# Kernel tuning notes

Measured on AMD Instinct MI355X. Metric: run time of the kernel, lower is better.

Reference implementation:

```python
import jax, jax.numpy as jnp
import numpy as np

N, E, F_IN, H, MH, C, G = 100000, 3200000, 128, 32, 64, 10, 64

def _seg_sum(data, ids, num):
    return jax.ops.segment_sum(data, ids, num_segments=num)

def gcn_conv(x, row, col, ew, W, b, n):
    # PyG GCNConv: linear first, then self-loops + symmetric edge-weight norm + scatter-add
    h = x @ W  # [N, H]
    loop = jnp.arange(n)
    r = jnp.concatenate([row, loop])
    c = jnp.concatenate([col, loop])
    w = jnp.concatenate([ew, jnp.ones((n,), dtype=ew.dtype)])
    deg = _seg_sum(w, c, n)
    dinv = jnp.where(deg > 0, jax.lax.rsqrt(deg), 0.0)
    norm = dinv[r] * w * dinv[c]  # [E+N]
    out = _seg_sum(norm[:, None] * h[r], c, n)  # scatter to targets
    return out + b

def setup_inputs():
    key = jax.random.key(0)
    ks = jax.random.split(key, 16)
    inp = {
        "x": jax.random.normal(ks[0], (N, F_IN), dtype=jnp.float32),
        "edge_index": jax.random.randint(ks[1], (2, E), 0, N, dtype=jnp.int64),
        "edge_weight": jax.random.uniform(ks[2], (E,), dtype=jnp.float32),
        "batch": jnp.sort(jax.random.randint(ks[3], (N,), 0, G, dtype=jnp.int64)),
    }
    def lin(k, i, o):
        s = 1.0 / np.sqrt(i)
        k1, k2 = jax.random.split(k)
        return (jax.random.uniform(k1, (i, o), minval=-s, maxval=s, dtype=jnp.float32),
                jax.random.uniform(k2, (o,), minval=-s, maxval=s, dtype=jnp.float32))
    inp["W1"], inp["b1"] = lin(ks[4], F_IN, H)
    inp["W2"], inp["b2"] = lin(ks[5], H, H)
    inp["W3"], inp["b3"] = lin(ks[6], H, H)
    inp["Wm0"], inp["bm0"] = lin(ks[7], H, MH)
    inp["Wm1"], inp["bm1"] = lin(ks[8], MH, MH)
    inp["Wout"], inp["bout"] = lin(ks[9], MH, C)
    return inp

def reference(x, edge_index, edge_weight, batch, W1, b1, W2, b2, W3, b3, Wm0, bm0, Wm1, bm1, Wout, bout):
    row, col = edge_index[0], edge_index[1]
    h = jax.nn.relu(gcn_conv(x, row, col, edge_weight, W1, b1, N))
    h = jax.nn.relu(gcn_conv(h, row, col, edge_weight, W2, b2, N))
    h = gcn_conv(h, row, col, edge_weight, W3, b3, N)
    # global mean pool over graphs
    sums = _seg_sum(h, batch, G)
    counts = _seg_sum(jnp.ones((N,), dtype=h.dtype), batch, G)
    g = sums / jnp.maximum(counts, 1.0)[:, None]
    # dropout p=0.5 is identity at inference (training=False)
    g = jax.nn.relu(g @ Wm0 + bm0)
    g = jax.nn.relu(g @ Wm1 + bm1)
    return g @ Wout + bout
```

## Files before the change

### kernel.cpp

```cpp
#include <hip/hip_runtime.h>

#define NN 100000
#define NE 3200000
#define FIN 128
#define HID 32
#define MH  64
#define NC  10
#define NG  64
#define NBKT 782
#define NBLK 512
#define EPB  (NE / NBLK)
#define SCANL (NBKT * NBLK)
#define SRCMASK 0x1FFFF
#define BCAP 5120

typedef float floatx2 __attribute__((ext_vector_type(2)));

__global__ __launch_bounds__(1024)
void hist_bkt(const int* __restrict__ ei, int* __restrict__ cnt2) {
    __shared__ int h[NBKT];
    int tid = threadIdx.x, blk = blockIdx.x;
    for (int b = tid; b < NBKT; b += 1024) h[b] = 0;
    __syncthreads();
    int base = blk * EPB;
    for (int i = tid; i < EPB; i += 1024)
        atomicAdd(&h[ei[NE + base + i] >> 7], 1);
    __syncthreads();
    for (int b = tid; b < NBKT; b += 1024) cnt2[b * NBLK + blk] = h[b];
}

__global__ void scan_block(const int* __restrict__ in, int* __restrict__ out,
                           int* __restrict__ bsum, int n) {
    __shared__ int lds[256];
    int tid = threadIdx.x;
    int base = blockIdx.x * 1024 + tid * 4;
    int v0 = 0, v1 = 0, v2 = 0, v3 = 0;
    if (base + 0 < n) v0 = in[base + 0];
    if (base + 1 < n) v1 = in[base + 1];
    if (base + 2 < n) v2 = in[base + 2];
    if (base + 3 < n) v3 = in[base + 3];
    int s = v0 + v1 + v2 + v3;
    lds[tid] = s;
    __syncthreads();
    for (int off = 1; off < 256; off <<= 1) {
        int val = (tid >= off) ? lds[tid - off] : 0;
        __syncthreads();
        lds[tid] += val;
        __syncthreads();
    }
    int excl = lds[tid] - s;
    if (tid == 255) bsum[blockIdx.x] = lds[255];
    if (base + 0 < n) out[base + 0] = excl;
    if (base + 1 < n) out[base + 1] = excl + v0;
    if (base + 2 < n) out[base + 2] = excl + v0 + v1;
    if (base + 3 < n) out[base + 3] = excl + v0 + v1 + v2;
}

__global__ void scan_top(int* __restrict__ bsum, int nb, float* __restrict__ sc) {
    int lane = threadIdx.x;
    for (int i = lane; i < NG * HID + NG; i += 64) sc[i] = 0.0f;
    int carry = 0;
    for (int base = 0; base < nb; base += 64) {
        int i = base + lane;
        int orig = (i < nb) ? bsum[i] : 0;
        int v = orig;
#pragma unroll
        for (int off = 1; off < 64; off <<= 1) {
            int t = __shfl_up(v, off, 64);
            if (lane >= off) v += t;
        }
        if (i < nb) bsum[i] = carry + v - orig;
        carry += __shfl(v, 63, 64);
    }
}

__global__ void scan_add(int* __restrict__ data, const int* __restrict__ bsum, int n) {
    int i = blockIdx.x * 256 + threadIdx.x;
    if (i < n) data[i] += bsum[i >> 10];
}

__global__ __launch_bounds__(1024)
void scatter_bkt(const int* __restrict__ ei, const float* __restrict__ ew,
                 const int* __restrict__ cnt2, const int* __restrict__ scanned,
                 int2* __restrict__ tre) {
    __shared__ int2 pay[EPB];
    __shared__ int scur[NBKT];
    __shared__ int hexc[NBKT];
    __shared__ int gbase[NBKT];
    int tid = threadIdx.x, blk = blockIdx.x;
    int myh = 0;
    if (tid < NBKT) {
        myh = cnt2[tid * NBLK + blk];
        gbase[tid] = scanned[tid * NBLK + blk];
        scur[tid] = myh;
    }
    __syncthreads();
    for (int off = 1; off < NBKT; off <<= 1) {
        int v = (tid < NBKT && tid >= off) ? scur[tid - off] : 0;
        __syncthreads();
        if (tid < NBKT) scur[tid] += v;
        __syncthreads();
    }
    if (tid < NBKT) { int ex = scur[tid] - myh; hexc[tid] = ex; scur[tid] = ex; }
    __syncthreads();
    int base = blk * EPB;
    for (int i = tid; i < EPB; i += 1024) {
        int e = base + i;
        int c = ei[NE + e];
        int r = ei[e];
        unsigned int wb = __float_as_uint(ew[e]);
        int b = c >> 7;
        int j = atomicAdd(&scur[b], 1);
        pay[j] = make_int2(r | ((c & 127) << 17) | ((b & 0xFF) << 24),
                           (int)((wb & ~3u) | ((unsigned)b >> 8)));
    }
    __syncthreads();
    for (int j = tid; j < EPB; j += 1024) {
        int2 q = pay[j];
        int b = (int)((((unsigned)q.y & 3u) << 8) | (((unsigned)q.x >> 24) & 0xFFu));
        int pos = gbase[b] + (j - hexc[b]);
        tre[pos] = make_int2(q.x & 0x00FFFFFF, q.y & ~3);
    }
}

__global__ __launch_bounds__(512)
void sort_k(const int2* __restrict__ tre, const int* __restrict__ scanned,
            unsigned int* __restrict__ srn4, int* __restrict__ rowptr,
            float* __restrict__ dinv) {
    __shared__ int2 ed[BCAP];
    __shared__ int h[128];
    __shared__ float dw[128];
    __shared__ int cur[128];
    int b = blockIdx.x, tid = threadIdx.x;
    int base = scanned[b * NBLK];
    int end = (b == NBKT - 1) ? NE : scanned[(b + 1) * NBLK];
    int n = end - base;
    bool staged = (n <= BCAP);
    if (tid < 128) { h[tid] = 0; dw[tid] = 0.f; }
    __syncthreads();
    for (int i = tid; i < n; i += 512) {
        int2 q = tre[base + i];
        if (staged) ed[i] = q;
        int key = (q.x >> 17) & 127;
        atomicAdd(&h[key], 1);
        atomicAdd(&dw[key], __int_as_float(q.y));
    }
    __syncthreads();
    if (tid < 64) {
        int lane = tid;
        int carry = 0;
#pragma unroll
        for (int c = 0; c < 2; ++c) {
            int idx = c * 64 + lane;
            int hv = h[idx];
            int v = hv;
#pragma unroll
            for (int off = 1; off < 64; off <<= 1) {
                int t = __shfl_up(v, off, 64);
                if (lane >= off) v += t;
            }
            cur[idx] = base + carry + v - hv;
            int node = b * 128 + idx;
            if (node < NN) {
                rowptr[node] = base + carry + v;
                dinv[node] = rsqrtf(1.0f + dw[idx]);
            }
            carry += __shfl(v, 63, 64);
        }
    }
    __syncthreads();
    for (int i = tid; i < n; i += 512) {
        int2 q = staged ? ed[i] : tre[base + i];
        int key = (q.x >> 17) & 127;
        int pos = atomicAdd(&cur[key], 1);
        unsigned int wb = (unsigned)q.y;
        wb += 0x7FFFu + ((wb >> 16) & 1u);
        srn4[pos] = (unsigned)(q.x & SRCMASK) | (((wb >> 16) & 0x7FFFu) << 17);
    }
}

template <int IN_DIM, bool RELU_IN>
__global__ __launch_bounds__(256)
void linear_k(const float* __restrict__ in, const float* __restrict__ W,
              const float* __restrict__ dinv, unsigned int* __restrict__ tmp8) {
    constexpr int J4 = IN_DIM / 4;
    constexpr int XSS = J4 + 1;
    __shared__ float4 xs[64 * XSS];
    __shared__ float4 wp[IN_DIM * 8];
    int tid = threadIdx.x;
    for (int idx = tid; idx < IN_DIM * 8; idx += 256) {
        int j = idx >> 3, kg = idx & 7;
        const float* wr = W + j * 32 + kg * 4;
        wp[idx] = make_float4(wr[0], wr[1], wr[2], wr[3]);
    }
    int rbase = blockIdx.x * 64;
    const float4* in4 = (const float4*)in;
    for (int idx = tid; idx < 64 * J4; idx += 256) {
        int row = idx / J4, j4 = idx % J4;
        int grow = rbase + row;
        float4 v = (grow < NN) ? in4[(size_t)grow * J4 + j4]
                               : make_float4(0.f, 0.f, 0.f, 0.f);
        if (RELU_IN) {
            v.x = fmaxf(v.x, 0.f); v.y = fmaxf(v.y, 0.f);
            v.z = fmaxf(v.z, 0.f); v.w = fmaxf(v.w, 0.f);
        }
        xs[row * XSS + j4] = v;
    }
    __syncthreads();
    int kg = tid & 7;
    int rp = tid >> 3;
    int r0 = rbase + 2 * rp;
    if (r0 >= NN) return;
    const float4* x0 = &xs[(2 * rp) * XSS];
    const float4* x1 = &xs[(2 * rp + 1) * XSS];
    float a00 = 0, a01 = 0, a02 = 0, a03 = 0;
    float a10 = 0, a11 = 0, a12 = 0, a13 = 0;
#pragma unroll
    for (int j4 = 0; j4 < J4; ++j4) {
        float4 v0 = x0[j4], v1 = x1[j4];
        const float4* wj = &wp[j4 * 4 * 8 + kg];
        float4 w0 = wj[0], w1 = wj[8], w2 = wj[16], w3 = wj[24];
#define LSTEP(VX0, VX1, W4) \
        a00 = fmaf(VX0, W4.x, a00); a01 = fmaf(VX0, W4.y, a01); \
        a02 = fmaf(VX0, W4.z, a02); a03 = fmaf(VX0, W4.w, a03); \
        a10 = fmaf(VX1, W4.x, a10); a11 = fmaf(VX1, W4.y, a11); \
        a12 = fmaf(VX1, W4.z, a12); a13 = fmaf(VX1, W4.w, a13);
        LSTEP(v0.x, v1.x, w0)
        LSTEP(v0.y, v1.y, w1)
        LSTEP(v0.z, v1.z, w2)
        LSTEP(v0.w, v1.w, w3)
#undef LSTEP
    }
    float d0 = dinv[r0], d1 = dinv[r0 + 1];
    a00 *= d0; a01 *= d0; a02 *= d0; a03 *= d0;
    a10 *= d1; a11 *= d1; a12 *= d1; a13 *= d1;
    int q0 = __builtin_amdgcn_cvt_pk_fp8_f32(a00, a01, 0, false);
    q0 = __builtin_amdgcn_cvt_pk_fp8_f32(a02, a03, q0, true);
    int q1 = __builtin_amdgcn_cvt_pk_fp8_f32(a10, a11, 0, false);
    q1 = __builtin_amdgcn_cvt_pk_fp8_f32(a12, a13, q1, true);
    tmp8[r0 * 8 + kg] = (unsigned int)q0;
    tmp8[(r0 + 1) * 8 + kg] = (unsigned int)q1;
}

struct AccR { floatx2 r0, r1, r2, r3, r4, r5, r6, r7; };

#define ACC8(A0,A1,A2,A3,A4,A5,A6,A7, U, W) { \
    floatx2 lo_, hi_; \
    lo_ = __builtin_amdgcn_cvt_pk_f32_fp8(U.x, false); \
    hi_ = __builtin_amdgcn_cvt_pk_f32_fp8(U.x, true); \
    A0 += lo_ * W; A1 += hi_ * W; \
    lo_ = __builtin_amdgcn_cvt_pk_f32_fp8(U.y, false); \
    hi_ = __builtin_amdgcn_cvt_pk_f32_fp8(U.y, true); \
    A2 += lo_ * W; A3 += hi_ * W; \
    lo_ = __builtin_amdgcn_cvt_pk_f32_fp8(U.z, false); \
    hi_ = __builtin_amdgcn_cvt_pk_f32_fp8(U.z, true); \
    A4 += lo_ * W; A5 += hi_ * W; \
    lo_ = __builtin_amdgcn_cvt_pk_f32_fp8(U.w, false); \
    hi_ = __builtin_amdgcn_cvt_pk_f32_fp8(U.w, true); \
    A6 += lo_ * W; A7 += hi_ * W; }

__device__ __forceinline__ AccR agg_core(const unsigned int* __restrict__ srn4,
                                         const int* __restrict__ rowptr,
                                         const unsigned int* __restrict__ tmp8,
                                         int nid, int s, unsigned int cb) {
    const char* t8 = (const char*)tmp8;
    int end = rowptr[nid];
    int start = (nid == 0) ? 0 : rowptr[nid - 1];
    floatx2 a0 = {0.f,0.f}, a1 = {0.f,0.f}, a2 = {0.f,0.f}, a3 = {0.f,0.f};
    floatx2 a4 = {0.f,0.f}, a5 = {0.f,0.f}, a6 = {0.f,0.f}, a7 = {0.f,0.f};
    floatx2 b0 = {0.f,0.f}, b1 = {0.f,0.f}, b2 = {0.f,0.f}, b3 = {0.f,0.f};
    floatx2 b4 = {0.f,0.f}, b5 = {0.f,0.f}, b6 = {0.f,0.f}, b7 = {0.f,0.f};
    int e = start + s;
    for (; e + 24 < end; e += 32) {
        unsigned int p0 = srn4[e];
        unsigned int p1 = srn4[e + 8];
        unsigned int p2 = srn4[e + 16];
        unsigned int p3 = srn4[e + 24];
        uint4 u0 = *(const uint4*)(t8 + (((p0 & SRCMASK) << 5) | cb));
        uint4 u1 = *(const uint4*)(t8 + (((p1 & SRCMASK) << 5) | cb));
        uint4 u2 = *(const uint4*)(t8 + (((p2 & SRCMASK) << 5) | cb));
        uint4 u3 = *(const uint4*)(t8 + (((p3 & SRCMASK) << 5) | cb));
        float w0 = __uint_as_float((p0 >> 1) & 0x7FFF0000u);
        float w1 = __uint_as_float((p1 >> 1) & 0x7FFF0000u);
        float w2 = __uint_as_float((p2 >> 1) & 0x7FFF0000u);
        float w3 = __uint_as_float((p3 >> 1) & 0x7FFF0000u);
        ACC8(a0,a1,a2,a3,a4,a5,a6,a7, u0, w0)
        ACC8(b0,b1,b2,b3,b4,b5,b6,b7, u1, w1)
        ACC8(a0,a1,a2,a3,a4,a5,a6,a7, u2, w2)
        ACC8(b0,b1,b2,b3,b4,b5,b6,b7, u3, w3)
    }
    for (; e < end; e += 8) {
        unsigned int p = srn4[e];
        uint4 u = *(const uint4*)(t8 + (((p & SRCMASK) << 5) | cb));
        float w = __uint_as_float((p >> 1) & 0x7FFF0000u);
        ACC8(a0,a1,a2,a3,a4,a5,a6,a7, u, w)
    }
    a0 += b0; a1 += b1; a2 += b2; a3 += b3;
    a4 += b4; a5 += b5; a6 += b6; a7 += b7;
#define REDM(M) { \
    a0.x += __shfl_xor(a0.x, M, 64); a0.y += __shfl_xor(a0.y, M, 64); \
    a1.x += __shfl_xor(a1.x, M, 64); a1.y += __shfl_xor(a1.y, M, 64); \
    a2.x += __shfl_xor(a2.x, M, 64); a2.y += __shfl_xor(a2.y, M, 64); \
    a3.x += __shfl_xor(a3.x, M, 64); a3.y += __shfl_xor(a3.y, M, 64); \
    a4.x += __shfl_xor(a4.x, M, 64); a4.y += __shfl_xor(a4.y, M, 64); \
    a5.x += __shfl_xor(a5.x, M, 64); a5.y += __shfl_xor(a5.y, M, 64); \
    a6.x += __shfl_xor(a6.x, M, 64); a6.y += __shfl_xor(a6.y, M, 64); \
    a7.x += __shfl_xor(a7.x, M, 64); a7.y += __shfl_xor(a7.y, M, 64); }
    REDM(2) REDM(4) REDM(8)
#undef REDM
    AccR r;
    r.r0 = a0; r.r1 = a1; r.r2 = a2; r.r3 = a3;
    r.r4 = a4; r.r5 = a5; r.r6 = a6; r.r7 = a7;
    return r;
}

#define EPILOGUE16(O0,O1,O2,O3, NID, CB, D, BIAS, A, RELU) { \
    const char* t8_ = (const char*)tmp8; \
    uint4 sv_ = *(const uint4*)(t8_ + (((unsigned)(NID)) << 5) + (CB)); \
    floatx2 s0_ = __builtin_amdgcn_cvt_pk_f32_fp8(sv_.x, false); \
    floatx2 s1_ = __builtin_amdgcn_cvt_pk_f32_fp8(sv_.x, true); \
    floatx2 s2_ = __builtin_amdgcn_cvt_pk_f32_fp8(sv_.y, false); \
    floatx2 s3_ = __builtin_amdgcn_cvt_pk_f32_fp8(sv_.y, true); \
    floatx2 s4_ = __builtin_amdgcn_cvt_pk_f32_fp8(sv_.z, false); \
    floatx2 s5_ = __builtin_amdgcn_cvt_pk_f32_fp8(sv_.z, true); \
    floatx2 s6_ = __builtin_amdgcn_cvt_pk_f32_fp8(sv_.w, false); \
    floatx2 s7_ = __builtin_amdgcn_cvt_pk_f32_fp8(sv_.w, true); \
    const float4* bp_ = (const float4*)(BIAS) + 4 * c; \
    float4 bq0_ = bp_[0], bq1_ = bp_[1], bq2_ = bp_[2], bq3_ = bp_[3]; \
    O0.x = bq0_.x + (D) * (s0_.x + A.r0.x); \
    O0.y = bq0_.y + (D) * (s0_.y + A.r0.y); \
    O0.z = bq0_.z + (D) * (s1_.x + A.r1.x); \
    O0.w = bq0_.w + (D) * (s1_.y + A.r1.y); \
    O1.x = bq1_.x + (D) * (s2_.x + A.r2.x); \
    O1.y = bq1_.y + (D) * (s2_.y + A.r2.y); \
    O1.z = bq1_.z + (D) * (s3_.x + A.r3.x); \
    O1.w = bq1_.w + (D) * (s3_.y + A.r3.y); \
    O2.x = bq2_.x + (D) * (s4_.x + A.r4.x); \
    O2.y = bq2_.y + (D) * (s4_.y + A.r4.y); \
    O2.z = bq2_.z + (D) * (s5_.x + A.r5.x); \
    O2.w = bq2_.w + (D) * (s5_.y + A.r5.y); \
    O3.x = bq3_.x + (D) * (s6_.x + A.r6.x); \
    O3.y = bq3_.y + (D) * (s6_.y + A.r6.y); \
    O3.z = bq3_.z + (D) * (s7_.x + A.r7.x); \
    O3.w = bq3_.w + (D) * (s7_.y + A.r7.y); \
    if (RELU) { \
        O0.x = fmaxf(O0.x, 0.f); O0.y = fmaxf(O0.y, 0.f); \
        O0.z = fmaxf(O0.z, 0.f); O0.w = fmaxf(O0.w, 0.f); \
        O1.x = fmaxf(O1.x, 0.f); O1.y = fmaxf(O1.y, 0.f); \
        O1.z = fmaxf(O1.z, 0.f); O1.w = fmaxf(O1.w, 0.f); \
        O2.x = fmaxf(O2.x, 0.f); O2.y = fmaxf(O2.y, 0.f); \
        O2.z = fmaxf(O2.z, 0.f); O2.w = fmaxf(O2.w, 0.f); \
        O3.x = fmaxf(O3.x, 0.f); O3.y = fmaxf(O3.y, 0.f); \
        O3.z = fmaxf(O3.z, 0.f); O3.w = fmaxf(O3.w, 0.f); \
    } }

__global__ __launch_bounds__(256)
void aggregate(const unsigned int* __restrict__ srn4,
               const int* __restrict__ rowptr,
               const float* __restrict__ dinv,
               const float* __restrict__ bias,
               const unsigned int* __restrict__ tmp8,
               float* __restrict__ h) {
    int tid = threadIdx.x;
    int nid = (blockIdx.x * 256 + tid) >> 4;
    int lane = tid & 63;
    int c = lane & 1, s = (lane >> 1) & 7;
    unsigned int cb = (unsigned int)c * 16u;
    AccR A = agg_core(srn4, rowptr, tmp8, nid, s, cb);
    if ((lane & 14) == 0) {
        float d = dinv[nid];
        float4 o0, o1, o2, o3;
        EPILOGUE16(o0, o1, o2, o3, nid, cb, d, bias, A, false)
        float4* hp = (float4*)(h + (size_t)nid * HID + 16 * c);
        hp[0] = o0; hp[1] = o1; hp[2] = o2; hp[3] = o3;
    }
}

__global__ __launch_bounds__(256)
void agg_lin(const unsigned int* __restrict__ srn4,
             const int* __restrict__ rowptr,
             const float* __restrict__ dinv,
             const float* __restrict__ bias,
             const float* __restrict__ Wn,
             const unsigned int* __restrict__ tmp8,
             unsigned int* __restrict__ tmp8_out) {
    __shared__ float hrow[4][4][HID];
    __shared__ float Wt[32][36];
    int tid = threadIdx.x;
    for (int idx = tid; idx < 1024; idx += 256)
        Wt[idx & 31][idx >> 5] = Wn[idx];
    int nid = (blockIdx.x * 256 + tid) >> 4;
    int wv = tid >> 6;
    int lane = tid & 63;
    int n = (lane >> 4) & 3;
    int c = lane & 1, s = (lane >> 1) & 7;
    unsigned int cb = (unsigned int)c * 16u;
    __syncthreads();
    AccR A = agg_core(srn4, rowptr, tmp8, nid, s, cb);
    float d = dinv[nid];
    if ((lane & 14) == 0) {
        float4 o0, o1, o2, o3;
        EPILOGUE16(o0, o1, o2, o3, nid, cb, d, bias, A, true)
        float4* hp = (float4*)&hrow[wv][n][16 * c];
        hp[0] = o0; hp[1] = o1; hp[2] = o2; hp[3] = o3;
    }
    int j0 = lane & 15;
    const float4* hb = (const float4*)&hrow[wv][n][0];
    float4 h0 = hb[0], h1 = hb[1], h2 = hb[2], h3 = hb[3];
    float4 h4 = hb[4], h5 = hb[5], h6 = hb[6], h7 = hb[7];
    const float4* w0p = (const float4*)&Wt[j0][0];
    const float4* w1p = (const float4*)&Wt[j0 + 16][0];
    float y0 = 0.f, y1 = 0.f;
#define MVSTEP(K, HV) { float4 wa_ = w0p[K]; float4 wb_ = w1p[K]; \
    y0 = fmaf(HV.x, wa_.x, y0); y0 = fmaf(HV.y, wa_.y, y0); \
    y0 = fmaf(HV.z, wa_.z, y0); y0 = fmaf(HV.w, wa_.w, y0); \
    y1 = fmaf(HV.x, wb_.x, y1); y1 = fmaf(HV.y, wb_.y, y1); \
    y1 = fmaf(HV.z, wb_.z, y1); y1 = fmaf(HV.w, wb_.w, y1); }
    MVSTEP(0, h0) MVSTEP(1, h1) MVSTEP(2, h2) MVSTEP(3, h3)
    MVSTEP(4, h4) MVSTEP(5, h5) MVSTEP(6, h6) MVSTEP(7, h7)
#undef MVSTEP
    y0 *= d; y1 *= d;
    float p1 = __shfl_down(y0, 1, 64);
    float p2 = __shfl_down(y0, 2, 64);
    float p3 = __shfl_down(y0, 3, 64);
    float q1 = __shfl_down(y1, 1, 64);
    float q2 = __shfl_down(y1, 2, 64);
    float q3 = __shfl_down(y1, 3, 64);
    if ((j0 & 3) == 0) {
        int t = j0 >> 2;
        int w0 = __builtin_amdgcn_cvt_pk_fp8_f32(y0, p1, 0, false);
        w0 = __builtin_amdgcn_cvt_pk_fp8_f32(p2, p3, w0, true);
        int w1 = __builtin_amdgcn_cvt_pk_fp8_f32(y1, q1, 0, false);
        w1 = __builtin_amdgcn_cvt_pk_fp8_f32(q2, q3, w1, true);
        tmp8_out[nid * 8 + t] = (unsigned int)w0;
        tmp8_out[nid * 8 + 4 + t] = (unsigned int)w1;
    }
}

__global__ void pool_k(const float* __restrict__ h, const int* __restrict__ batch,
                       float* __restrict__ sums, float* __restrict__ counts) {
    int t = blockIdx.x * 256 + threadIdx.x;
    int chunk = t >> 5, k = t & 31;
    int n0 = chunk * 32;
    if (n0 >= NN) return;
    int n1 = min(n0 + 32, NN);
    int g = batch[n0];
    float acc = 0.f, cacc = 0.f;
    for (int i = n0; i < n1; ++i) {
        int gi = batch[i];
        if (gi != g) {
            atomicAdd(&sums[g * HID + k], acc);
            if (k == 0) atomicAdd(&counts[g], cacc);
            g = gi; acc = 0.f; cacc = 0.f;
        }
        acc += h[(size_t)i * HID + k];
        cacc += 1.f;
    }
    atomicAdd(&sums[g * HID + k], acc);
    if (k == 0) atomicAdd(&counts[g], cacc);
}

__global__ __launch_bounds__(64)
void mlp_k(const float* __restrict__ sums, const float* __restrict__ counts,
           const float* __restrict__ Wm0, const float* __restrict__ bm0,
           const float* __restrict__ Wm1, const float* __restrict__ bm1,
           const float* __restrict__ Wout, const float* __restrict__ bout,
           float* __restrict__ out) {
    __shared__ float g0[HID];
    __shared__ float g1[MH];
    __shared__ float g2[MH];
    int g = blockIdx.x;
    int k = threadIdx.x;
    if (k < HID) g0[k] = sums[g * HID + k] / fmaxf(counts[g], 1.0f);
    __syncthreads();
    float acc = bm0[k];
#pragma unroll
    for (int j = 0; j < HID; ++j) acc = fmaf(g0[j], Wm0[j * MH + k], acc);
    g1[k] = fmaxf(acc, 0.f);
    __syncthreads();
    float acc2 = bm1[k];
#pragma unroll
    for (int j = 0; j < MH; ++j) acc2 = fmaf(g1[j], Wm1[j * MH + k], acc2);
    g2[k] = fmaxf(acc2, 0.f);
    __syncthreads();
    if (k < NC) {
        float acc3 = bout[k];
#pragma unroll
        for (int j = 0; j < MH; ++j) acc3 = fmaf(g2[j], Wout[j * NC + k], acc3);
        out[g * NC + k] = acc3;
    }
}

extern "C" void kernel_launch(void* const* d_in, const int* in_sizes, int n_in,
                              void* d_out, int out_size, void* d_ws, size_t ws_size,
                              hipStream_t stream) {
    const float* x    = (const float*)d_in[0];
    const int*   ei   = (const int*)d_in[1];
    const float* ew   = (const float*)d_in[2];
    const int*   batch= (const int*)d_in[3];
    const float* W1   = (const float*)d_in[4];
    const float* b1   = (const float*)d_in[5];
    const float* W2   = (const float*)d_in[6];
    const float* b2   = (const float*)d_in[7];
    const float* W3   = (const float*)d_in[8];
    const float* b3   = (const float*)d_in[9];
    const float* Wm0  = (const float*)d_in[10];
    const float* bm0  = (const float*)d_in[11];
    const float* Wm1  = (const float*)d_in[12];
    const float* bm1  = (const float*)d_in[13];
    const float* Wout = (const float*)d_in[14];
    const float* bout = (const float*)d_in[15];
    float* out = (float*)d_out;

    char* p = (char*)d_ws;
    unsigned int* srn4 = (unsigned int*)p; p += sizeof(unsigned int) * (size_t)NE;
    char*  S   = p;                      p += 12 * (size_t)NE;
    int2*  tre = (int2*)S;
    int*   cnt2    = (int*)(S + sizeof(int2) * (size_t)NE);
    int*   scanned = cnt2 + SCANL;
    unsigned int* tmp8  = (unsigned int*)S;
    unsigned int* tmp8b = tmp8 + (size_t)NN * 8;
    float* hA  = (float*)(S + 2 * (size_t)NN * HID);
    int*   bsum    = (int*)p;            p += sizeof(int) * 512;
    float* dinv    = (float*)p;          p += sizeof(float) * NN;
    int*   rowptr  = (int*)p;            p += sizeof(int) * NN;
    float* sums    = (float*)p;          p += sizeof(float) * NG * HID;
    float* counts  = (float*)p;

    dim3 blk(256);
    const int NB_SCAN = (SCANL + 1023) / 1024;
    const int NB_LIN = (NN + 63) / 64;
    const int NB_AGG = 6250;

    hist_bkt<<<NBLK, 1024, 0, stream>>>(ei, cnt2);
    scan_block<<<NB_SCAN, blk, 0, stream>>>(cnt2, scanned, bsum, SCANL);
    scan_top<<<1, 64, 0, stream>>>(bsum, NB_SCAN, sums);
    scan_add<<<(SCANL + 255) / 256, blk, 0, stream>>>(scanned, bsum, SCANL);
    scatter_bkt<<<NBLK, 1024, 0, stream>>>(ei, ew, cnt2, scanned, tre);
    sort_k<<<NBKT, 512, 0, stream>>>(tre, scanned, srn4, rowptr, dinv);

    linear_k<FIN, false><<<NB_LIN, blk, 0, stream>>>(x, W1, dinv, tmp8);
    agg_lin<<<NB_AGG, blk, 0, stream>>>(srn4, rowptr, dinv, b1, W2, tmp8, tmp8b);
    agg_lin<<<NB_AGG, blk, 0, stream>>>(srn4, rowptr, dinv, b2, W3, tmp8b, tmp8);
    aggregate<<<NB_AGG, blk, 0, stream>>>(srn4, rowptr, dinv, b3, tmp8, hA);

    pool_k<<<391, blk, 0, stream>>>(hA, batch, sums, counts);
    mlp_k<<<NG, 64, 0, stream>>>(sums, counts, Wm0, bm0, Wm1, bm1, Wout, bout, out);
}
```

Measured before the change: 372.5 us.

## Replace two-level bucket sort CSR build with global atomic counting sort

```diff
diff --git a/kernel.cpp b/kernel.cpp
--- a/kernel.cpp
+++ b/kernel.cpp
@@ -7,38 +7,40 @@
 #define MH  64
 #define NC  10
 #define NG  64
-#define NBKT 782
-#define NBLK 512
-#define EPB  (NE / NBLK)
-#define SCANL (NBKT * NBLK)
 #define SRCMASK 0x1FFFF
-#define BCAP 5120
 
 typedef float floatx2 __attribute__((ext_vector_type(2)));
 
-__global__ __launch_bounds__(1024)
-void hist_bkt(const int* __restrict__ ei, int* __restrict__ cnt2) {
-    __shared__ int h[NBKT];
-    int tid = threadIdx.x, blk = blockIdx.x;
-    for (int b = tid; b < NBKT; b += 1024) h[b] = 0;
-    __syncthreads();
-    int base = blk * EPB;
-    for (int i = tid; i < EPB; i += 1024)
-        atomicAdd(&h[ei[NE + base + i] >> 7], 1);
-    __syncthreads();
-    for (int b = tid; b < NBKT; b += 1024) cnt2[b * NBLK + blk] = h[b];
-}
-
-__global__ void scan_block(const int* __restrict__ in, int* __restrict__ out,
-                           int* __restrict__ bsum, int n) {
+
+__global__ __launch_bounds__(256)
+void zero_k(unsigned long long* __restrict__ cw) {
+    int i = blockIdx.x * 256 + threadIdx.x;
+    if (i < NN) cw[i] = 0ULL;
+}
+
+__global__ __launch_bounds__(256)
+void deg_k(const int* __restrict__ ei, const float* __restrict__ ew,
+           unsigned long long* __restrict__ cw) {
+    int stride = gridDim.x * 256;
+    for (int e = blockIdx.x * 256 + threadIdx.x; e < NE; e += stride) {
+        int c = ei[NE + e];
+        float w = ew[e];
+        unsigned long long add =
+            (1ULL << 40) | (unsigned long long)(w * 4294967296.0f);
+        atomicAdd(&cw[c], add);
+    }
+}
+
+__global__ void scan_cnt(const unsigned long long* __restrict__ cw,
+                         int* __restrict__ out, int* __restrict__ bsum, int n) {
     __shared__ int lds[256];
     int tid = threadIdx.x;
     int base = blockIdx.x * 1024 + tid * 4;
     int v0 = 0, v1 = 0, v2 = 0, v3 = 0;
-    if (base + 0 < n) v0 = in[base + 0];
-    if (base + 1 < n) v1 = in[base + 1];
-    if (base + 2 < n) v2 = in[base + 2];
-    if (base + 3 < n) v3 = in[base + 3];
+    if (base + 0 < n) v0 = (int)(cw[base + 0] >> 40);
+    if (base + 1 < n) v1 = (int)(cw[base + 1] >> 40);
+    if (base + 2 < n) v2 = (int)(cw[base + 2] >> 40);
+    if (base + 3 < n) v3 = (int)(cw[base + 3] >> 40);
     int s = v0 + v1 + v2 + v3;
     lds[tid] = s;
     __syncthreads();
@@ -74,108 +76,33 @@
     }
 }
 
-__global__ void scan_add(int* __restrict__ data, const int* __restrict__ bsum, int n) {
+__global__ __launch_bounds__(256)
+void scan_fin(const unsigned long long* __restrict__ cw,
+              const int* __restrict__ excl, const int* __restrict__ bsum,
+              int* __restrict__ cur, int* __restrict__ rowptr,
+              float* __restrict__ dinv) {
     int i = blockIdx.x * 256 + threadIdx.x;
-    if (i < n) data[i] += bsum[i >> 10];
-}
-
-__global__ __launch_bounds__(1024)
-void scatter_bkt(const int* __restrict__ ei, const float* __restrict__ ew,
-                 const int* __restrict__ cnt2, const int* __restrict__ scanned,
-                 int2* __restrict__ tre) {
-    __shared__ int2 pay[EPB];
-    __shared__ int scur[NBKT];
-    __shared__ int hexc[NBKT];
-    __shared__ int gbase[NBKT];
-    int tid = threadIdx.x, blk = blockIdx.x;
-    int myh = 0;
-    if (tid < NBKT) {
-        myh = cnt2[tid * NBLK + blk];
-        gbase[tid] = scanned[tid * NBLK + blk];
-        scur[tid] = myh;
-    }
-    __syncthreads();
-    for (int off = 1; off < NBKT; off <<= 1) {
-        int v = (tid < NBKT && tid >= off) ? scur[tid - off] : 0;
-        __syncthreads();
-        if (tid < NBKT) scur[tid] += v;
-        __syncthreads();
-    }
-    if (tid < NBKT) { int ex = scur[tid] - myh; hexc[tid] = ex; scur[tid] = ex; }
-    __syncthreads();
-    int base = blk * EPB;
-    for (int i = tid; i < EPB; i += 1024) {
-        int e = base + i;
+    if (i >= NN) return;
+    unsigned long long v = cw[i];
+    int cnt = (int)(v >> 40);
+    float ws = (float)(v & 0xFFFFFFFFFFULL) * (1.0f / 4294967296.0f);
+    int start = excl[i] + bsum[i >> 10];
+    cur[i] = start;
+    rowptr[i] = start + cnt;
+    dinv[i] = rsqrtf(1.0f + ws);
+}
+
+__global__ __launch_bounds__(256)
+void scatter_srn(const int* __restrict__ ei, const float* __restrict__ ew,
+                 int* __restrict__ cur, unsigned int* __restrict__ srn4) {
+    int stride = gridDim.x * 256;
+    for (int e = blockIdx.x * 256 + threadIdx.x; e < NE; e += stride) {
+        int r = ei[e];
         int c = ei[NE + e];
-        int r = ei[e];
         unsigned int wb = __float_as_uint(ew[e]);
-        int b = c >> 7;
-        int j = atomicAdd(&scur[b], 1);
-        pay[j] = make_int2(r | ((c & 127) << 17) | ((b & 0xFF) << 24),
-                           (int)((wb & ~3u) | ((unsigned)b >> 8)));
-    }
-    __syncthreads();
-    for (int j = tid; j < EPB; j += 1024) {
-        int2 q = pay[j];
-        int b = (int)((((unsigned)q.y & 3u) << 8) | (((unsigned)q.x >> 24) & 0xFFu));
-        int pos = gbase[b] + (j - hexc[b]);
-        tre[pos] = make_int2(q.x & 0x00FFFFFF, q.y & ~3);
-    }
-}
-
-__global__ __launch_bounds__(512)
-void sort_k(const int2* __restrict__ tre, const int* __restrict__ scanned,
-            unsigned int* __restrict__ srn4, int* __restrict__ rowptr,
-            float* __restrict__ dinv) {
-    __shared__ int2 ed[BCAP];
-    __shared__ int h[128];
-    __shared__ float dw[128];
-    __shared__ int cur[128];
-    int b = blockIdx.x, tid = threadIdx.x;
-    int base = scanned[b * NBLK];
-    int end = (b == NBKT - 1) ? NE : scanned[(b + 1) * NBLK];
-    int n = end - base;
-    bool staged = (n <= BCAP);
-    if (tid < 128) { h[tid] = 0; dw[tid] = 0.f; }
-    __syncthreads();
-    for (int i = tid; i < n; i += 512) {
-        int2 q = tre[base + i];
-        if (staged) ed[i] = q;
-        int key = (q.x >> 17) & 127;
-        atomicAdd(&h[key], 1);
-        atomicAdd(&dw[key], __int_as_float(q.y));
-    }
-    __syncthreads();
-    if (tid < 64) {
-        int lane = tid;
-        int carry = 0;
-#pragma unroll
-        for (int c = 0; c < 2; ++c) {
-            int idx = c * 64 + lane;
-            int hv = h[idx];
-            int v = hv;
-#pragma unroll
-            for (int off = 1; off < 64; off <<= 1) {
-                int t = __shfl_up(v, off, 64);
-                if (lane >= off) v += t;
-            }
-            cur[idx] = base + carry + v - hv;
-            int node = b * 128 + idx;
-            if (node < NN) {
-                rowptr[node] = base + carry + v;
-                dinv[node] = rsqrtf(1.0f + dw[idx]);
-            }
-            carry += __shfl(v, 63, 64);
-        }
-    }
-    __syncthreads();
-    for (int i = tid; i < n; i += 512) {
-        int2 q = staged ? ed[i] : tre[base + i];
-        int key = (q.x >> 17) & 127;
-        int pos = atomicAdd(&cur[key], 1);
-        unsigned int wb = (unsigned)q.y;
         wb += 0x7FFFu + ((wb >> 16) & 1u);
-        srn4[pos] = (unsigned)(q.x & SRCMASK) | (((wb >> 16) & 0x7FFFu) << 17);
+        int pos = atomicAdd(&cur[c], 1);
+        srn4[pos] = (unsigned)r | (((wb >> 16) & 0x7FFFu) << 17);
     }
 }
 
@@ -515,12 +442,12 @@
     char* p = (char*)d_ws;
     unsigned int* srn4 = (unsigned int*)p; p += sizeof(unsigned int) * (size_t)NE;
     char*  S   = p;                      p += 12 * (size_t)NE;
-    int2*  tre = (int2*)S;
-    int*   cnt2    = (int*)(S + sizeof(int2) * (size_t)NE);
-    int*   scanned = cnt2 + SCANL;
     unsigned int* tmp8  = (unsigned int*)S;
     unsigned int* tmp8b = tmp8 + (size_t)NN * 8;
     float* hA  = (float*)(S + 2 * (size_t)NN * HID);
+    unsigned long long* cw = (unsigned long long*)(S + 20 * 1024 * 1024);
+    int*   cur  = (int*)(S + 21 * 1024 * 1024);
+    int*   excl = (int*)(S + 22 * 1024 * 1024);
     int*   bsum    = (int*)p;            p += sizeof(int) * 512;
     float* dinv    = (float*)p;          p += sizeof(float) * NN;
     int*   rowptr  = (int*)p;            p += sizeof(int) * NN;
@@ -528,16 +455,18 @@
     float* counts  = (float*)p;
 
     dim3 blk(256);
-    const int NB_SCAN = (SCANL + 1023) / 1024;
+    const int NB_NODE = (NN + 255) / 256;
+    const int NB_SCAN = (NN + 1023) / 1024;
     const int NB_LIN = (NN + 63) / 64;
     const int NB_AGG = 6250;
-
-    hist_bkt<<<NBLK, 1024, 0, stream>>>(ei, cnt2);
-    scan_block<<<NB_SCAN, blk, 0, stream>>>(cnt2, scanned, bsum, SCANL);
+    const int NB_EDGE = 2048;
+
+    zero_k<<<NB_NODE, blk, 0, stream>>>(cw);
+    deg_k<<<NB_EDGE, blk, 0, stream>>>(ei, ew, cw);
+    scan_cnt<<<NB_SCAN, blk, 0, stream>>>(cw, excl, bsum, NN);
     scan_top<<<1, 64, 0, stream>>>(bsum, NB_SCAN, sums);
-    scan_add<<<(SCANL + 255) / 256, blk, 0, stream>>>(scanned, bsum, SCANL);
-    scatter_bkt<<<NBLK, 1024, 0, stream>>>(ei, ew, cnt2, scanned, tre);
-    sort_k<<<NBKT, 512, 0, stream>>>(tre, scanned, srn4, rowptr, dinv);
+    scan_fin<<<NB_NODE, blk, 0, stream>>>(cw, excl, bsum, cur, rowptr, dinv);
+    scatter_srn<<<NB_EDGE, blk, 0, stream>>>(ei, ew, cur, srn4);
 
     linear_k<FIN, false><<<NB_LIN, blk, 0, stream>>>(x, W1, dinv, tmp8);
     agg_lin<<<NB_AGG, blk, 0, stream>>>(srn4, rowptr, dinv, b1, W2, tmp8, tmp8b);
```

After: 699.4 us. +87.8%, slower.
